# Kernel tuning notes

Measured on AMD Instinct MI355X. Metric: run time of the kernel, lower is better.

Reference implementation:

```python
import jax, jax.numpy as jnp
import numpy as np

B, L, HID = 4, 1024, 1024
H, D = 16, 64  # num heads, head size


def setup_inputs() -> dict:
    key = jax.random.key(0)
    ks = jax.random.split(key, 12)
    s = 0.02
    return {
        "hidden_states": jax.random.normal(ks[0], (B, L, HID), jnp.float32),
        "attention_mask": jnp.zeros((B, 1, 1, L), jnp.float32),
        "structure_matrix": jax.random.normal(ks[1], (L, L, D), jnp.float32),
        # torch nn.Linear weights are [out, in]
        "Wq": jax.random.normal(ks[2], (H * D, HID), jnp.float32) * s,
        "bq": jnp.zeros((H * D,), jnp.float32),
        "Wk": jax.random.normal(ks[3], (H * D, HID), jnp.float32) * s,
        "bk": jnp.zeros((H * D,), jnp.float32),
        "Wv": jax.random.normal(ks[4], (H * D, HID), jnp.float32) * s,
        "bv": jnp.zeros((H * D,), jnp.float32),
        "Wsq": jax.random.normal(ks[5], (D, D), jnp.float32) * s,
        "bsq": jnp.zeros((D,), jnp.float32),
        "Wsk": jax.random.normal(ks[6], (D, D), jnp.float32) * s,
        "bsk": jnp.zeros((D,), jnp.float32),
    }


def _heads(x):
    # [B, L, H*D] -> [B, H, L, D]
    return x.reshape(B, L, H, D).transpose(0, 2, 1, 3)


def reference(hidden_states, attention_mask, structure_matrix,
              Wq, bq, Wk, bk, Wv, bv, Wsq, bsq, Wsk, bsk):
    q = _heads(hidden_states @ Wq.T + bq)  # [B,H,L,D]
    k = _heads(hidden_states @ Wk.T + bk)
    v = _heads(hidden_states @ Wv.T + bv)

    scores = jnp.einsum('bhld,bhrd->bhlr', q, k)

    sq = structure_matrix @ Wsq.T + bsq  # [L,L,D]
    sk = structure_matrix @ Wsk.T + bsk
    scores = scores + jnp.einsum('bhld,lrd->bhlr', q, sq) \
                    + jnp.einsum('bhrd,lrd->bhlr', k, sk)

    scores = scores / jnp.sqrt(jnp.float32(D)) + attention_mask
    probs = jax.nn.softmax(scores, axis=-1)
    ctx = jnp.einsum('bhlr,bhrd->bhld', probs, v)
    ctx = ctx.transpose(0, 2, 1, 3).reshape(B, L, H * D)
    return ctx, scores
```

## Files before the change

kernel.cpp:

```cpp
#include <hip/hip_runtime.h>

typedef __attribute__((ext_vector_type(8))) short short8v;
typedef __attribute__((ext_vector_type(4))) short short4v;
typedef __attribute__((ext_vector_type(4))) float float4v;

#define MFMA16(a,b,c) __builtin_amdgcn_mfma_f32_16x16x32_bf16(a,b,c,0,0,0)

__device__ __forceinline__ unsigned short f2b(float f) {
    union { float f; unsigned u; } v; v.f = f;
    unsigned r = v.u + 0x7FFFu + ((v.u >> 16) & 1u);
    return (unsigned short)(r >> 16);
}
__device__ __forceinline__ float b2f(unsigned short s) {
    union { unsigned u; float f; } v; v.u = ((unsigned)s) << 16;
    return v.f;
}
__device__ __forceinline__ short8v pack8(float4v a, float4v b) {
    short8v o;
    o[0]=(short)f2b(a[0]); o[1]=(short)f2b(a[1]); o[2]=(short)f2b(a[2]); o[3]=(short)f2b(a[3]);
    o[4]=(short)f2b(b[0]); o[5]=(short)f2b(b[1]); o[6]=(short)f2b(b[2]); o[7]=(short)f2b(b[3]);
    return o;
}

__global__ __launch_bounds__(256) void pack_bf16(
    const float* __restrict__ in, unsigned short* __restrict__ out, int n8) {
    int i = blockIdx.x * 256 + threadIdx.x;
    if (i < n8) {
        float4v a = *(const float4v*)&in[(size_t)i * 8];
        float4v b = *(const float4v*)&in[(size_t)i * 8 + 4];
        *(short8v*)&out[(size_t)i * 8] = pack8(a, b);
    }
}

__global__ __launch_bounds__(256) void qkv_gemm(
    const unsigned short* __restrict__ A,
    const unsigned short* __restrict__ W,
    const float* __restrict__ bias,
    unsigned short* __restrict__ out, int vmode) {
    const int wave = threadIdx.x >> 6, lane = threadIdx.x & 63;
    const int m0 = blockIdx.y * 128 + wave * 32;
    const int n0 = blockIdx.x * 64;
    const int lrow = lane & 15, g8 = (lane >> 4) << 3, row4 = (lane >> 4) << 2;
    float4v acc[2][4] = {};
    const unsigned short* Ap = A + (size_t)(m0 + lrow) * 1024 + g8;
    const unsigned short* Wp = W + (size_t)(n0 + lrow) * 1024 + g8;
#pragma unroll 2
    for (int k0 = 0; k0 < 1024; k0 += 32) {
        short8v a0 = *(const short8v*)(Ap + k0);
        short8v a1 = *(const short8v*)(Ap + 16 * 1024 + k0);
        short8v b0 = *(const short8v*)(Wp + k0);
        short8v b1 = *(const short8v*)(Wp + 16 * 1024 + k0);
        short8v b2 = *(const short8v*)(Wp + 32 * 1024 + k0);
        short8v b3 = *(const short8v*)(Wp + 48 * 1024 + k0);
        acc[0][0] = MFMA16(a0, b0, acc[0][0]); acc[0][1] = MFMA16(a0, b1, acc[0][1]);
        acc[0][2] = MFMA16(a0, b2, acc[0][2]); acc[0][3] = MFMA16(a0, b3, acc[0][3]);
        acc[1][0] = MFMA16(a1, b0, acc[1][0]); acc[1][1] = MFMA16(a1, b1, acc[1][1]);
        acc[1][2] = MFMA16(a1, b2, acc[1][2]); acc[1][3] = MFMA16(a1, b3, acc[1][3]);
    }
#pragma unroll
    for (int nt = 0; nt < 4; ++nt) {
        const int n = n0 + nt * 16 + lrow;
        const float bz = bias[n];
        const int h = n >> 6, d = n & 63;
#pragma unroll
        for (int mt = 0; mt < 2; ++mt) {
            const int mb = m0 + mt * 16 + row4;
            if (vmode == 0) {
#pragma unroll
                for (int j = 0; j < 4; ++j) {
                    const int m = mb + j;
                    const int b = m >> 10, l = m & 1023;
                    out[(((size_t)(b * 16 + h) << 10) + l) * 64 + d] = f2b(acc[mt][nt][j] + bz);
                }
            } else {
                const int b = mb >> 10, r = mb & 1023;
                short4v pk;
#pragma unroll
                for (int j = 0; j < 4; ++j) pk[j] = (short)f2b(acc[mt][nt][j] + bz);
                *(short4v*)&out[((((size_t)(b * 16 + h)) << 6) + d) * 1024 + r] = pk;
            }
        }
    }
}

__global__ __launch_bounds__(256) void headproj(
    const unsigned short* __restrict__ xh,
    const float* __restrict__ Wsx,
    const float* __restrict__ bsx,
    unsigned short* __restrict__ x2b,
    float* __restrict__ xbv) {
    __shared__ __align__(16) float Ws[64 * 64];
    __shared__ float bs[64];
    __shared__ __align__(16) unsigned short Xl[64 * 64];
    const int tid = threadIdx.x;
    const int l = blockIdx.x;
#pragma unroll
    for (int i = 0; i < 4; ++i)
        *(float4v*)&Ws[tid * 4 + i * 1024] = *(const float4v*)&Wsx[tid * 4 + i * 1024];
    if (tid < 64) bs[tid] = bsx[tid];
    {
        const int bhh = tid >> 2, dq = (tid & 3) * 16;
        const unsigned short* src = &xh[((size_t)bhh * 1024 + l) * 64 + dq];
        *(short8v*)&Xl[bhh * 64 + dq] = *(const short8v*)src;
        *(short8v*)&Xl[bhh * 64 + dq + 8] = *(const short8v*)(src + 8);
    }
    __syncthreads();
    const int bh = tid >> 2, e0 = (tid & 3) * 16;
    float acc[16] = {};
    float bacc = 0.f;
    for (int d = 0; d < 64; ++d) {
        const float xd = b2f(Xl[bh * 64 + d]);
        bacc += xd * bs[d];
        const float* wr = &Ws[d * 64 + e0];
#pragma unroll
        for (int e = 0; e < 16; e += 4) {
            float4v w = *(const float4v*)&wr[e];
            acc[e] += xd * w[0]; acc[e + 1] += xd * w[1];
            acc[e + 2] += xd * w[2]; acc[e + 3] += xd * w[3];
        }
    }
    short8v p0, p1;
#pragma unroll
    for (int e = 0; e < 8; ++e) { p0[e] = (short)f2b(acc[e]); p1[e] = (short)f2b(acc[e + 8]); }
    unsigned short* dst = &x2b[((size_t)l * 64 + bh) * 64 + e0];
    *(short8v*)dst = p0; *(short8v*)(dst + 8) = p1;
    if ((tid & 3) == 0) xbv[l * 64 + bh] = bacc;
}

__global__ __launch_bounds__(256, 3) void struct_fused(
    const unsigned short* __restrict__ Sb,
    const unsigned short* __restrict__ q2b,
    const unsigned short* __restrict__ k2b,
    const float* __restrict__ qbv,
    const float* __restrict__ kbv,
    unsigned short* __restrict__ sb) {
    __shared__ __align__(16) unsigned short Ssh[256 * 64];
    __shared__ __align__(16) unsigned short t3g[4][4][16][16];
    const int tid = threadIdx.x;
    const int w = tid >> 6, lane = tid & 63;
    const int lrow = lane & 15, g = lane >> 4;
    const int g8 = g << 3, row4 = g << 2;
    const int w16 = w << 4;
    const int r0 = blockIdx.x << 4, l0 = blockIdx.y << 4;

    {
        const int lrow8 = lane >> 3, lslot = lane & 7;
#pragma unroll
        for (int i = 0; i < 8; ++i) {
            const int row = (w << 6) + (i << 3) + lrow8;
            const int cg = lslot ^ ((row ^ (row >> 4)) & 7);
            const unsigned short* src =
                Sb + ((size_t)(l0 + (row >> 4)) * 1024 + r0 + (row & 15)) * 64 + (cg << 3);
            unsigned short* dst = (unsigned short*)Ssh + (size_t)((w << 6) + (i << 3)) * 64;
            __builtin_amdgcn_global_load_lds(
                (const __attribute__((address_space(1))) void*)src,
                (__attribute__((address_space(3))) void*)dst, 16, 0, 0);
        }
    }
    float kbreg[4];
#pragma unroll
    for (int j = 0; j < 4; ++j)
        kbreg[j] = kbv[(size_t)(r0 + row4 + j) * 64 + w16 + lrow];
    asm volatile("s_waitcnt vmcnt(0)" ::: "memory");
    __syncthreads();

    float4v c3[16];
#pragma unroll
    for (int ri = 0; ri < 16; ++ri) {
        const int row = lrow * 16 + ri;
        const int key = (lrow ^ ri) & 7;
        short8v a0 = *(const short8v*)&Ssh[row * 64 + ((g ^ key) << 3)];
        short8v a1 = *(const short8v*)&Ssh[row * 64 + (((4 + g) ^ key) << 3)];
        const unsigned short* Bp = k2b + ((size_t)(r0 + ri) * 64 + w16 + lrow) * 64 + g8;
        short8v b0 = *(const short8v*)Bp;
        short8v b1 = *(const short8v*)(Bp + 32);
        float4v acc = {};
        acc = MFMA16(a0, b0, acc);
        acc = MFMA16(a1, b1, acc);
        c3[ri] = acc;
    }

#pragma unroll
    for (int G = 0; G < 4; ++G) {
        if (g == G) {
#pragma unroll
            for (int j = 0; j < 4; ++j) {
                short8v lo, hi;
#pragma unroll
                for (int i = 0; i < 8; ++i) {
                    lo[i] = (short)f2b(c3[i][j]);
                    hi[i] = (short)f2b(c3[8 + i][j]);
                }
                *(short8v*)&t3g[w][j][lrow][0] = lo;
                *(short8v*)&t3g[w][j][lrow][8] = hi;
            }
        }
        asm volatile("s_waitcnt lgkmcnt(0)" ::: "memory");
#pragma unroll
        for (int lj = 0; lj < 4; ++lj) {
            const int li = (G << 2) + lj;
            const int row = li * 16 + lrow;
            const int key = (li ^ lrow) & 7;
            short8v a0 = *(const short8v*)&Ssh[row * 64 + ((g ^ key) << 3)];
            short8v a1 = *(const short8v*)&Ssh[row * 64 + (((4 + g) ^ key) << 3)];
            const unsigned short* Bp = q2b + ((size_t)(l0 + li) * 64 + w16 + lrow) * 64 + g8;
            short8v b0 = *(const short8v*)Bp;
            short8v b1 = *(const short8v*)(Bp + 32);
            float4v c2 = {};
            c2 = MFMA16(a0, b0, c2);
            c2 = MFMA16(a1, b1, c2);
            short4v t3v = *(const short4v*)&t3g[w][lj][lrow][row4];
            const float qb = qbv[(size_t)(l0 + li) * 64 + w16 + lrow];
            short4v outv;
#pragma unroll
            for (int j = 0; j < 4; ++j)
                outv[j] = (short)f2b(c2[j] + b2f((unsigned short)t3v[j]) + qb + kbreg[j]);
            *(short4v*)&sb[((size_t)(l0 + li) * 64 + w16 + lrow) * 1024 + r0 + row4] = outv;
        }
    }
}

__global__ __launch_bounds__(256) void flash_kernel(
    const unsigned short* __restrict__ qh,
    const unsigned short* __restrict__ kh,
    const unsigned short* __restrict__ vT,
    const unsigned short* __restrict__ sb,
    const float* __restrict__ mask,
    float* __restrict__ scores,
    float* __restrict__ ctx) {
    __shared__ __align__(16) float scL[32 * 64];
    __shared__ __align__(16) unsigned short pL[32 * 64];
    __shared__ float mL[32], sL[32], fL[32];
    const int bid = blockIdx.x;
    const int virt = (bid & 7) * 256 + (bid >> 3);
    const int bh = virt >> 5, lt = virt & 31;
    const int b = bh >> 4, h = bh & 15, l0 = lt * 32;
    const int tid = threadIdx.x, wave = tid >> 6, lane = tid & 63;
    const int lrow = lane & 15, g8 = (lane >> 4) << 3, row4 = (lane >> 4) << 2;
    short8v qf[2][2];
#pragma unroll
    for (int mt = 0; mt < 2; ++mt)
#pragma unroll
        for (int ks = 0; ks < 2; ++ks)
            qf[mt][ks] = *(const short8v*)&qh[((size_t)bh * 1024 + l0 + mt * 16 + lrow) * 64 + ks * 32 + g8];
    float4v opv[2] = {};
    if (tid < 32) { mL[tid] = -3e38f; sL[tid] = 0.f; }
    __syncthreads();
    const int tl = tid >> 3, tr8 = tid & 7;
    const int keyS = ((tl >> 2) & 3) << 4;
    const int keyP = (tl & 7) << 3;
    for (int rt = 0; rt < 16; ++rt) {
        const int r0 = rt * 64;
        float4v sacc[2] = {};
#pragma unroll
        for (int ks = 0; ks < 2; ++ks) {
            short8v kf = *(const short8v*)&kh[((size_t)bh * 1024 + r0 + wave * 16 + lrow) * 64 + ks * 32 + g8];
            sacc[0] = MFMA16(qf[0][ks], kf, sacc[0]);
            sacc[1] = MFMA16(qf[1][ks], kf, sacc[1]);
        }
#pragma unroll
        for (int mt = 0; mt < 2; ++mt)
#pragma unroll
            for (int j = 0; j < 4; ++j) {
                const int ll = mt * 16 + row4 + j;
                const int cc = wave * 16 + lrow;
                scL[ll * 64 + (cc ^ (((ll >> 2) & 3) << 4))] = sacc[mt][j];
            }
        __syncthreads();
        float4v x0 = *(const float4v*)&scL[tl * 64 + ((tr8 * 8) ^ keyS)];
        float4v x1 = *(const float4v*)&scL[tl * 64 + ((tr8 * 8 + 4) ^ keyS)];
        short8v sbv = *(const short8v*)&sb[((size_t)(l0 + tl) * 64 + bh) * 1024 + r0 + tr8 * 8];
        float4v mk0 = *(const float4v*)&mask[(size_t)b * 1024 + r0 + tr8 * 8];
        float4v mk1 = *(const float4v*)&mask[(size_t)b * 1024 + r0 + tr8 * 8 + 4];
        float s8[8];
#pragma unroll
        for (int i = 0; i < 4; ++i) {
            s8[i]     = (x0[i] + b2f((unsigned short)sbv[i])) * 0.125f + mk0[i];
            s8[i + 4] = (x1[i] + b2f((unsigned short)sbv[i + 4])) * 0.125f + mk1[i];
        }
        {
            float4v o0, o1;
#pragma unroll
            for (int i = 0; i < 4; ++i) { o0[i] = s8[i]; o1[i] = s8[i + 4]; }
            float* sgp = &scores[((size_t)bh * 1024 + l0 + tl) * 1024 + r0 + tr8 * 8];
            *(float4v*)sgp = o0; *(float4v*)(sgp + 4) = o1;
        }
        float tm = s8[0];
#pragma unroll
        for (int i = 1; i < 8; ++i) tm = fmaxf(tm, s8[i]);
        tm = fmaxf(tm, __shfl_xor(tm, 1));
        tm = fmaxf(tm, __shfl_xor(tm, 2));
        tm = fmaxf(tm, __shfl_xor(tm, 4));
        const float mold = mL[tl];
        const float mnew = fmaxf(mold, tm);
        const float f = __expf(mold - mnew);
        float psum = 0.f;
        float p8[8];
#pragma unroll
        for (int i = 0; i < 8; ++i) { p8[i] = __expf(s8[i] - mnew); psum += p8[i]; }
        psum += __shfl_xor(psum, 1);
        psum += __shfl_xor(psum, 2);
        psum += __shfl_xor(psum, 4);
        if (tr8 == 0) { sL[tl] = sL[tl] * f + psum; mL[tl] = mnew; fL[tl] = f; }
        short8v pk;
#pragma unroll
        for (int i = 0; i < 8; ++i) pk[i] = (short)f2b(p8[i]);
        *(short8v*)&pL[tl * 64 + ((tr8 * 8) ^ keyP)] = pk;
        __syncthreads();
#pragma unroll
        for (int mt = 0; mt < 2; ++mt)
#pragma unroll
            for (int j = 0; j < 4; ++j) opv[mt][j] *= fL[mt * 16 + row4 + j];
#pragma unroll
        for (int ks = 0; ks < 2; ++ks) {
            short8v pf0 = *(const short8v*)&pL[(lrow) * 64 + ((ks * 32 + g8) ^ ((lrow & 7) << 3))];
            short8v pf1 = *(const short8v*)&pL[(16 + lrow) * 64 + ((ks * 32 + g8) ^ ((lrow & 7) << 3))];
            short8v vf = *(const short8v*)&vT[((size_t)bh * 64 + wave * 16 + lrow) * 1024 + r0 + ks * 32 + g8];
            opv[0] = MFMA16(pf0, vf, opv[0]);
            opv[1] = MFMA16(pf1, vf, opv[1]);
        }
    }
#pragma unroll
    for (int mt = 0; mt < 2; ++mt)
#pragma unroll
        for (int j = 0; j < 4; ++j) {
            const int l = mt * 16 + row4 + j;
            const float inv = 1.f / sL[l];
            const int d = wave * 16 + lrow;
            ctx[((size_t)b * 1024 + l0 + l) * 1024 + h * 64 + d] = opv[mt][j] * inv;
        }
}

extern "C" void kernel_launch(void* const* d_in, const int* in_sizes, int n_in,
                              void* d_out, int out_size, void* d_ws, size_t ws_size,
                              hipStream_t stream) {
    (void)in_sizes; (void)n_in; (void)out_size; (void)ws_size;
    const float* hidden = (const float*)d_in[0];
    const float* mask   = (const float*)d_in[1];
    const float* S      = (const float*)d_in[2];
    const float* Wq  = (const float*)d_in[3];  const float* bq  = (const float*)d_in[4];
    const float* Wk  = (const float*)d_in[5];  const float* bk  = (const float*)d_in[6];
    const float* Wv  = (const float*)d_in[7];  const float* bv  = (const float*)d_in[8];
    const float* Wsq = (const float*)d_in[9];  const float* bsq = (const float*)d_in[10];
    const float* Wsk = (const float*)d_in[11]; const float* bsk = (const float*)d_in[12];

    float* ctx    = (float*)d_out;
    float* scores = ctx + (size_t)4 * 1024 * 1024;

    char* ws = (char*)d_ws;
    unsigned short* sbuf = (unsigned short*)ws;
    unsigned short* hb  = (unsigned short*)ws;
    unsigned short* Wqb = (unsigned short*)(ws + (8u << 20));
    unsigned short* Wkb = (unsigned short*)(ws + (10u << 20));
    unsigned short* Wvb = (unsigned short*)(ws + (12u << 20));
    unsigned short* qh  = (unsigned short*)(ws + (size_t)(128u) * 1024 * 1024);
    unsigned short* kh  = qh  + (size_t)4 * 1024 * 1024;
    unsigned short* vT  = kh  + (size_t)4 * 1024 * 1024;
    unsigned short* q2b = vT  + (size_t)4 * 1024 * 1024;
    unsigned short* k2b = q2b + (size_t)4 * 1024 * 1024;
    float* qbv = (float*)(k2b + (size_t)4 * 1024 * 1024);
    float* kbv = qbv + 65536;
    unsigned short* Sbuf = (unsigned short*)scores;

    pack_bf16<<<2048, 256, 0, stream>>>(hidden, hb, 524288);
    pack_bf16<<<512, 256, 0, stream>>>(Wq, Wqb, 131072);
    pack_bf16<<<512, 256, 0, stream>>>(Wk, Wkb, 131072);
    pack_bf16<<<512, 256, 0, stream>>>(Wv, Wvb, 131072);
    pack_bf16<<<32768, 256, 0, stream>>>(S, Sbuf, 8388608);
    qkv_gemm<<<dim3(16, 32), 256, 0, stream>>>(hb, Wqb, bq, qh, 0);
    qkv_gemm<<<dim3(16, 32), 256, 0, stream>>>(hb, Wkb, bk, kh, 0);
    qkv_gemm<<<dim3(16, 32), 256, 0, stream>>>(hb, Wvb, bv, vT, 1);
    headproj<<<1024, 256, 0, stream>>>(qh, Wsq, bsq, q2b, qbv);
    headproj<<<1024, 256, 0, stream>>>(kh, Wsk, bsk, k2b, kbv);
    struct_fused<<<dim3(64, 64), 256, 0, stream>>>(Sbuf, q2b, k2b, qbv, kbv, sbuf);
    flash_kernel<<<2048, 256, 0, stream>>>(qh, kh, vT, sbuf, mask, scores, ctx);
}
```

Measured before the change: 603.3 us.

## Read fp32 structure matrix directly in struct_fused and merge pack kernels

Removes the separate pass that converted the 256 MB fp32 structure matrix to bf16. struct_fused now streams fp32 rows straight into LDS and converts them to bf16 at fragment-load time with the hardware packed-convert instruction. The small pack launches for hidden and the Q/K/V weights are merged into one kernel. The cost is that LDS use in struct_fused doubles (occupancy hint lowered from 3 to 2 blocks per CU), and rounding now relies on the native cvt instruction.

```diff
diff --git a/kernel.cpp b/kernel.cpp
--- a/kernel.cpp
+++ b/kernel.cpp
@@ -16,20 +16,28 @@
     return v.f;
 }
 __device__ __forceinline__ short8v pack8(float4v a, float4v b) {
-    short8v o;
-    o[0]=(short)f2b(a[0]); o[1]=(short)f2b(a[1]); o[2]=(short)f2b(a[2]); o[3]=(short)f2b(a[3]);
-    o[4]=(short)f2b(b[0]); o[5]=(short)f2b(b[1]); o[6]=(short)f2b(b[2]); o[7]=(short)f2b(b[3]);
-    return o;
-}
-
-__global__ __launch_bounds__(256) void pack_bf16(
-    const float* __restrict__ in, unsigned short* __restrict__ out, int n8) {
-    int i = blockIdx.x * 256 + threadIdx.x;
-    if (i < n8) {
-        float4v a = *(const float4v*)&in[(size_t)i * 8];
-        float4v b = *(const float4v*)&in[(size_t)i * 8 + 4];
-        *(short8v*)&out[(size_t)i * 8] = pack8(a, b);
-    }
+    union { unsigned u[4]; short8v s; } o;
+    asm("v_cvt_pk_bf16_f32 %0, %1, %2" : "=v"(o.u[0]) : "v"(a[0]), "v"(a[1]));
+    asm("v_cvt_pk_bf16_f32 %0, %1, %2" : "=v"(o.u[1]) : "v"(a[2]), "v"(a[3]));
+    asm("v_cvt_pk_bf16_f32 %0, %1, %2" : "=v"(o.u[2]) : "v"(b[0]), "v"(b[1]));
+    asm("v_cvt_pk_bf16_f32 %0, %1, %2" : "=v"(o.u[3]) : "v"(b[2]), "v"(b[3]));
+    return o.s;
+}
+
+__global__ __launch_bounds__(256) void pack_all(
+    const float* __restrict__ hidden, const float* __restrict__ Wq,
+    const float* __restrict__ Wk, const float* __restrict__ Wv,
+    unsigned short* __restrict__ hb, unsigned short* __restrict__ Wqb,
+    unsigned short* __restrict__ Wkb, unsigned short* __restrict__ Wvb) {
+    const int bid = blockIdx.x;
+    const float* in; unsigned short* out; int i;
+    if (bid < 2048)      { in = hidden; out = hb;  i = bid * 256 + threadIdx.x; }
+    else if (bid < 2560) { in = Wq; out = Wqb; i = (bid - 2048) * 256 + threadIdx.x; }
+    else if (bid < 3072) { in = Wk; out = Wkb; i = (bid - 2560) * 256 + threadIdx.x; }
+    else                 { in = Wv; out = Wvb; i = (bid - 3072) * 256 + threadIdx.x; }
+    float4v a = *(const float4v*)&in[(size_t)i * 8];
+    float4v b = *(const float4v*)&in[(size_t)i * 8 + 4];
+    *(short8v*)&out[(size_t)i * 8] = pack8(a, b);
 }
 
 __global__ __launch_bounds__(256) void qkv_gemm(
@@ -127,14 +135,14 @@
     if ((tid & 3) == 0) xbv[l * 64 + bh] = bacc;
 }
 
-__global__ __launch_bounds__(256, 3) void struct_fused(
-    const unsigned short* __restrict__ Sb,
+__global__ __launch_bounds__(256, 2) void struct_fused(
+    const float* __restrict__ S,
     const unsigned short* __restrict__ q2b,
     const unsigned short* __restrict__ k2b,
     const float* __restrict__ qbv,
     const float* __restrict__ kbv,
     unsigned short* __restrict__ sb) {
-    __shared__ __align__(16) unsigned short Ssh[256 * 64];
+    __shared__ __align__(16) float Ssh[256 * 64];
     __shared__ __align__(16) unsigned short t3g[4][4][16][16];
     const int tid = threadIdx.x;
     const int w = tid >> 6, lane = tid & 63;
@@ -144,14 +152,15 @@
     const int r0 = blockIdx.x << 4, l0 = blockIdx.y << 4;
 
     {
-        const int lrow8 = lane >> 3, lslot = lane & 7;
-#pragma unroll
-        for (int i = 0; i < 8; ++i) {
-            const int row = (w << 6) + (i << 3) + lrow8;
-            const int cg = lslot ^ ((row ^ (row >> 4)) & 7);
-            const unsigned short* src =
-                Sb + ((size_t)(l0 + (row >> 4)) * 1024 + r0 + (row & 15)) * 64 + (cg << 3);
-            unsigned short* dst = (unsigned short*)Ssh + (size_t)((w << 6) + (i << 3)) * 64;
+        const int rowoff = lane >> 4, c = lane & 15;
+#pragma unroll
+        for (int i = 0; i < 16; ++i) {
+            const int row = (w << 6) + (i << 2) + rowoff;
+            const int key = (row ^ (row >> 4)) & 7;
+            const int sc = ((((c >> 1) ^ key) << 1) | (c & 1));
+            const float* src =
+                S + ((size_t)(l0 + (row >> 4)) * 1024 + r0 + (row & 15)) * 64 + (sc << 2);
+            float* dst = Ssh + (size_t)((w << 6) + (i << 2)) * 64;
             __builtin_amdgcn_global_load_lds(
                 (const __attribute__((address_space(1))) void*)src,
                 (__attribute__((address_space(3))) void*)dst, 16, 0, 0);
@@ -169,8 +178,10 @@
     for (int ri = 0; ri < 16; ++ri) {
         const int row = lrow * 16 + ri;
         const int key = (lrow ^ ri) & 7;
-        short8v a0 = *(const short8v*)&Ssh[row * 64 + ((g ^ key) << 3)];
-        short8v a1 = *(const short8v*)&Ssh[row * 64 + (((4 + g) ^ key) << 3)];
+        const float* pr = Ssh + row * 64;
+        const int p0 = (g ^ key) << 3, p1 = ((4 + g) ^ key) << 3;
+        short8v a0 = pack8(*(const float4v*)(pr + p0), *(const float4v*)(pr + p0 + 4));
+        short8v a1 = pack8(*(const float4v*)(pr + p1), *(const float4v*)(pr + p1 + 4));
         const unsigned short* Bp = k2b + ((size_t)(r0 + ri) * 64 + w16 + lrow) * 64 + g8;
         short8v b0 = *(const short8v*)Bp;
         short8v b1 = *(const short8v*)(Bp + 32);
@@ -186,11 +197,11 @@
 #pragma unroll
             for (int j = 0; j < 4; ++j) {
                 short8v lo, hi;
-#pragma unroll
-                for (int i = 0; i < 8; ++i) {
-                    lo[i] = (short)f2b(c3[i][j]);
-                    hi[i] = (short)f2b(c3[8 + i][j]);
-                }
+                float4v la{c3[0][j], c3[1][j], c3[2][j], c3[3][j]};
+                float4v lb{c3[4][j], c3[5][j], c3[6][j], c3[7][j]};
+                float4v ha{c3[8][j], c3[9][j], c3[10][j], c3[11][j]};
+                float4v hb{c3[12][j], c3[13][j], c3[14][j], c3[15][j]};
+                lo = pack8(la, lb); hi = pack8(ha, hb);
                 *(short8v*)&t3g[w][j][lrow][0] = lo;
                 *(short8v*)&t3g[w][j][lrow][8] = hi;
             }
@@ -201,8 +212,10 @@
             const int li = (G << 2) + lj;
             const int row = li * 16 + lrow;
             const int key = (li ^ lrow) & 7;
-            short8v a0 = *(const short8v*)&Ssh[row * 64 + ((g ^ key) << 3)];
-            short8v a1 = *(const short8v*)&Ssh[row * 64 + (((4 + g) ^ key) << 3)];
+            const float* pr = Ssh + row * 64;
+            const int p0 = (g ^ key) << 3, p1 = ((4 + g) ^ key) << 3;
+            short8v a0 = pack8(*(const float4v*)(pr + p0), *(const float4v*)(pr + p0 + 4));
+            short8v a1 = pack8(*(const float4v*)(pr + p1), *(const float4v*)(pr + p1 + 4));
             const unsigned short* Bp = q2b + ((size_t)(l0 + li) * 64 + w16 + lrow) * 64 + g8;
             short8v b0 = *(const short8v*)Bp;
             short8v b1 = *(const short8v*)(Bp + 32);
@@ -360,18 +373,13 @@
     unsigned short* k2b = q2b + (size_t)4 * 1024 * 1024;
     float* qbv = (float*)(k2b + (size_t)4 * 1024 * 1024);
     float* kbv = qbv + 65536;
-    unsigned short* Sbuf = (unsigned short*)scores;
-
-    pack_bf16<<<2048, 256, 0, stream>>>(hidden, hb, 524288);
-    pack_bf16<<<512, 256, 0, stream>>>(Wq, Wqb, 131072);
-    pack_bf16<<<512, 256, 0, stream>>>(Wk, Wkb, 131072);
-    pack_bf16<<<512, 256, 0, stream>>>(Wv, Wvb, 131072);
-    pack_bf16<<<32768, 256, 0, stream>>>(S, Sbuf, 8388608);
+
+    pack_all<<<3584, 256, 0, stream>>>(hidden, Wq, Wk, Wv, hb, Wqb, Wkb, Wvb);
     qkv_gemm<<<dim3(16, 32), 256, 0, stream>>>(hb, Wqb, bq, qh, 0);
     qkv_gemm<<<dim3(16, 32), 256, 0, stream>>>(hb, Wkb, bk, kh, 0);
     qkv_gemm<<<dim3(16, 32), 256, 0, stream>>>(hb, Wvb, bv, vT, 1);
     headproj<<<1024, 256, 0, stream>>>(qh, Wsq, bsq, q2b, qbv);
     headproj<<<1024, 256, 0, stream>>>(kh, Wsk, bsk, k2b, kbv);
-    struct_fused<<<dim3(64, 64), 256, 0, stream>>>(Sbuf, q2b, k2b, qbv, kbv, sbuf);
+    struct_fused<<<dim3(64, 64), 256, 0, stream>>>(S, q2b, k2b, qbv, kbv, sbuf);
     flash_kernel<<<2048, 256, 0, stream>>>(qh, kh, vT, sbuf, mask, scores, ctx);
 }
```

Measured after the change: 535.9 us. -11.2%, faster.
